# Kernel optimization log

Hardware: AMD Instinct MI355X
Metric: run time of the kernel (lower is better)

The kernel has to match this reference:

```python
import jax, jax.numpy as jnp
import numpy as np

N_HEADS = 16
EMBED = 1024
SEQ = 2048
BATCH = 4
GELU_C = 0.044715
EPS = 1e-5


def gelu_tanh(x):
    return 0.5 * x * (1.0 + jnp.tanh(jnp.sqrt(2.0 / jnp.pi) * (x + GELU_C * x ** 3)))


def layer_norm(x, scale, shift):
    mean = jnp.mean(x, axis=-1, keepdims=True)
    var = jnp.var(x, axis=-1, keepdims=True)
    return scale * (x - mean) / jnp.sqrt(var + EPS) + shift


def setup_inputs() -> dict:
    key = jax.random.key(0)
    ks = jax.random.split(key, 8)
    d = EMBED
    s = 0.02
    return {
        "X": jax.random.normal(ks[0], (BATCH, SEQ, d), dtype=jnp.float32),
        "Wq": jax.random.normal(ks[1], (d, d), dtype=jnp.float32) * s,
        "Wk": jax.random.normal(ks[2], (d, d), dtype=jnp.float32) * s,
        "Wv": jax.random.normal(ks[3], (d, d), dtype=jnp.float32) * s,
        "Wo": jax.random.normal(ks[4], (d, d), dtype=jnp.float32) * s,
        "W1": jax.random.normal(ks[5], (d, 4 * d), dtype=jnp.float32) * s,
        "b1": jnp.zeros((4 * d,), dtype=jnp.float32),
        "W2": jax.random.normal(ks[6], (4 * d, d), dtype=jnp.float32) * s,
        "b2": jnp.zeros((d,), dtype=jnp.float32),
        "ln1_scale": jnp.ones((d,), dtype=jnp.float32),
        "ln1_shift": jnp.zeros((d,), dtype=jnp.float32),
        "ln2_scale": jnp.ones((d,), dtype=jnp.float32),
        "ln2_shift": jnp.zeros((d,), dtype=jnp.float32),
    }


def attention(x, Wq, Wk, Wv, Wo):
    b, s, d = x.shape
    h, dh = N_HEADS, d // N_HEADS
    q = (x @ Wq).reshape(b, s, h, dh).transpose(0, 2, 1, 3)  # [b,h,s,dh]
    k = (x @ Wk).reshape(b, s, h, dh).transpose(0, 2, 1, 3)
    v = (x @ Wv).reshape(b, s, h, dh).transpose(0, 2, 1, 3)
    scores = jnp.einsum("bhqd,bhkd->bhqk", q, k) / jnp.sqrt(jnp.float32(dh))
    causal = jnp.tril(jnp.ones((s, s), dtype=bool))
    scores = jnp.where(causal, scores, -jnp.inf)
    w = jax.nn.softmax(scores, axis=-1)  # dropout rate 0 -> identity
    ctx = jnp.einsum("bhqk,bhkd->bhqd", w, v)
    ctx = ctx.transpose(0, 2, 1, 3).reshape(b, s, d)
    return ctx @ Wo


def reference(X, Wq, Wk, Wv, Wo, W1, b1, W2, b2,
              ln1_scale, ln1_shift, ln2_scale, ln2_shift):
    h = layer_norm(X, ln1_scale, ln1_shift)
    X = X + attention(h, Wq, Wk, Wv, Wo)
    h = layer_norm(X, ln2_scale, ln2_shift)
    h = gelu_tanh(h @ W1 + b1) @ W2 + b2
    return X + h
```

## Files before the change

### kernel.cpp

```cpp
#include <hip/hip_runtime.h>

typedef unsigned short u16;
typedef __attribute__((ext_vector_type(8))) short bf16x8;
typedef __attribute__((ext_vector_type(4))) float fx4;

#define MFMA16(a, b, c) __builtin_amdgcn_mfma_f32_16x16x32_bf16((a), (b), (c), 0, 0, 0)

__device__ __forceinline__ u16 f2bf(float f) {
  unsigned u = __float_as_uint(f);
  u += 0x7fffu + ((u >> 16) & 1u);
  return (u16)(u >> 16);
}

__device__ __forceinline__ void gload_lds16(const void* g, void* l) {
  __builtin_amdgcn_global_load_lds((const __attribute__((address_space(1))) void*)g,
                                   (__attribute__((address_space(3))) void*)l,
                                   16, 0, 0);
}

struct WP {
  const float* s[6];
  u16* d[6];
};
__global__ __launch_bounds__(256) void tcvt_all(WP p) {
  __shared__ float t[32][33];
  const int id = blockIdx.x;
  int which, bx, by, R, C;
  if (id < 4096) {
    which = id >> 10;
    const int q = id & 1023;
    bx = q >> 5; by = q & 31; R = 1024; C = 1024;
  } else if (id < 8192) {
    which = 4;
    const int q = id - 4096;
    bx = q & 127; by = q >> 7; R = 1024; C = 4096;
  } else {
    which = 5;
    const int q = id - 8192;
    bx = q & 31; by = q >> 5; R = 4096; C = 1024;
  }
  const float* src = p.s[which];
  u16* dst = p.d[which];
  const int tx = threadIdx.x & 31, ty = threadIdx.x >> 5;
#pragma unroll
  for (int i = 0; i < 4; ++i)
    t[ty + i * 8][tx] = src[(size_t)(by * 32 + ty + i * 8) * C + bx * 32 + tx];
  __syncthreads();
#pragma unroll
  for (int i = 0; i < 4; ++i)
    dst[(size_t)(bx * 32 + ty + i * 8) * R + by * 32 + tx] = f2bf(t[tx][ty + i * 8]);
}

__global__ __launch_bounds__(256) void ln_kernel(const float* __restrict__ x,
                                                 const float* __restrict__ sc,
                                                 const float* __restrict__ sh,
                                                 u16* __restrict__ out) {
  const int row = blockIdx.x, tid = threadIdx.x;
  const float4 v = ((const float4*)(x + (size_t)row * 1024))[tid];
  float s = v.x + v.y + v.z + v.w;
  float ss = v.x * v.x + v.y * v.y + v.z * v.z + v.w * v.w;
#pragma unroll
  for (int d = 32; d >= 1; d >>= 1) {
    s += __shfl_xor(s, d);
    ss += __shfl_xor(ss, d);
  }
  __shared__ float rs[4], rq[4];
  const int w = tid >> 6;
  if ((tid & 63) == 0) { rs[w] = s; rq[w] = ss; }
  __syncthreads();
  s = rs[0] + rs[1] + rs[2] + rs[3];
  ss = rq[0] + rq[1] + rq[2] + rq[3];
  const float mean = s * (1.f / 1024.f);
  const float var = ss * (1.f / 1024.f) - mean * mean;
  const float rstd = rsqrtf(var + 1e-5f);
  const float4 g = ((const float4*)sc)[tid];
  const float4 b = ((const float4*)sh)[tid];
  ushort4 o;
  o.x = f2bf(g.x * (v.x - mean) * rstd + b.x);
  o.y = f2bf(g.y * (v.y - mean) * rstd + b.y);
  o.z = f2bf(g.z * (v.z - mean) * rstd + b.z);
  o.w = f2bf(g.w * (v.w - mean) * rstd + b.w);
  ((ushort4*)(out + (size_t)row * 1024))[tid] = o;
}

__device__ __forceinline__ void xcd_map(int bid, int NTN, int& tMi, int& tNi) {
  const int xcd = bid & 7, i = bid >> 3;
  tMi = xcd + 8 * (i / NTN);
  tNi = i % NTN;
}

template <int MODE>
__global__ __launch_bounds__(256) void gemm_bf16(
    const u16* __restrict__ A, const u16* __restrict__ Bt, int K, int NTN,
    void* __restrict__ outp, const float* __restrict__ aux,
    u16* __restrict__ qd, u16* __restrict__ kd, u16* __restrict__ vd) {
  __shared__ u16 lA[128 * 32];
  __shared__ u16 lB[128 * 32];
  const int tid = threadIdx.x;
  const int w = tid >> 6, lane = tid & 63;
  const int lo = lane & 15, hi = lane >> 4;
  int tMi, tNi;
  xcd_map(blockIdx.x, NTN, tMi, tNi);
  const int tM = tMi * 128, tN = tNi * 128;
  const int wr = (w >> 1) << 6, wc = (w & 1) << 6;

  const u16 *sA[2], *sB[2];
  u16 *dA[2], *dB[2];
#pragma unroll
  for (int p = 0; p < 2; ++p) {
    const int c = p * 256 + tid;
    const int r = c >> 2, gs = (c & 3) ^ (r & 3);
    sA[p] = A + (size_t)(tM + r) * K + gs * 8;
    sB[p] = Bt + (size_t)(tN + r) * K + gs * 8;
    dA[p] = &lA[(p * 256 + w * 64) * 8];
    dB[p] = &lB[(p * 256 + w * 64) * 8];
  }

  fx4 acc[4][4];
#pragma unroll
  for (int m = 0; m < 4; ++m)
#pragma unroll
    for (int n = 0; n < 4; ++n) acc[m][n] = (fx4){0.f, 0.f, 0.f, 0.f};

  for (int kk = 0; kk < K; kk += 32) {
    __syncthreads();
#pragma unroll
    for (int p = 0; p < 2; ++p) {
      gload_lds16(sA[p] + kk, dA[p]);
      gload_lds16(sB[p] + kk, dB[p]);
    }
    __syncthreads();
    bf16x8 af[4], bfr[4];
#pragma unroll
    for (int m = 0; m < 4; ++m) {
      const int r = wr + m * 16 + lo;
      af[m] = *(const bf16x8*)&lA[r * 32 + ((hi ^ (r & 3)) << 3)];
    }
#pragma unroll
    for (int n = 0; n < 4; ++n) {
      const int r = wc + n * 16 + lo;
      bfr[n] = *(const bf16x8*)&lB[r * 32 + ((hi ^ (r & 3)) << 3)];
    }
#pragma unroll
    for (int m = 0; m < 4; ++m)
#pragma unroll
      for (int n = 0; n < 4; ++n) acc[m][n] = MFMA16(af[m], bfr[n], acc[m][n]);
  }

#pragma unroll
  for (int m = 0; m < 4; ++m) {
    const int rgb = tM + wr + m * 16 + hi * 4;
#pragma unroll
    for (int n = 0; n < 4; ++n) {
      const int cg = tN + wc + n * 16 + lo;
#pragma unroll
      for (int r = 0; r < 4; ++r) {
        const float v = acc[m][n][r];
        const int rg = rgb + r;
        if constexpr (MODE == 0) {
          const int which = cg >> 10, c = cg & 1023;
          const int head = c >> 6, dhi = c & 63;
          const int b = rg >> 11, sidx = rg & 2047;
          const int bh = b * 16 + head;
          const u16 bv = f2bf(v);
          if (which == 0)      qd[((size_t)bh * 2048 + sidx) * 64 + dhi] = bv;
          else if (which == 1) kd[((size_t)bh * 2048 + sidx) * 64 + dhi] = bv;
          else                 vd[((size_t)bh * 64 + dhi) * 2048 + sidx] = bv;
        } else if constexpr (MODE == 1) {
          float* o = (float*)outp;
          const size_t idx = (size_t)rg * 1024 + cg;
          o[idx] = aux[idx] + v;
        } else if constexpr (MODE == 2) {
          const float xx = v + aux[cg];
          const float t = xx + 0.044715f * xx * xx * xx;
          const float e = __expf(1.5957691216057308f * t);
          const float th = 1.f - 2.f / (e + 1.f);
          ((u16*)outp)[(size_t)rg * 4096 + cg] = f2bf(0.5f * xx * (1.f + th));
        } else {
          float* o = (float*)outp;
          const size_t idx = (size_t)rg * 1024 + cg;
          o[idx] = o[idx] + v + aux[cg];
        }
      }
    }
  }
}

__global__ __launch_bounds__(512) void attn_kernel(const u16* __restrict__ Q,
                                                   const u16* __restrict__ Kg,
                                                   const u16* __restrict__ Vt,
                                                   u16* __restrict__ ctx) {
  __shared__ u16 lK[2][64 * 64];
  __shared__ u16 lV[2][64 * 64];
  __shared__ u16 Plds[8][16 * 64];
  const int tid = threadIdx.x;
  const int w = tid >> 6, lane = tid & 63;
  const int lo = lane & 15, hi = lane >> 4;
  const int bh = blockIdx.x;
  const int j = blockIdx.y;
  const u16* Qb = Q + (size_t)bh * 2048 * 64;
  const u16* Kb = Kg + (size_t)bh * 2048 * 64;
  const u16* Vb = Vt + (size_t)bh * 64 * 2048;
  u16* Pw = Plds[w];
  const int nt0 = 2 * j + 2;

  const int rowS = tid >> 3;
  const int ugS = (tid & 7) ^ (rowS & 7);

#define STAGE(BUF, KB)                                                         \
  do {                                                                         \
    gload_lds16(Kb + (size_t)((KB) + rowS) * 64 + ugS * 8, &lK[BUF][tid * 8]); \
    gload_lds16(Vb + (size_t)rowS * 2048 + (KB) + ugS * 8, &lV[BUF][tid * 8]); \
  } while (0)

  const int b = bh >> 4, h = bh & 15;
  const float SCALE = 0.18033688011112042f;

  bf16x8 ones;
#pragma unroll
  for (int i = 0; i < 8; ++i) ones[i] = (short)0x3F80;

  int qt = j;
  int qw = qt * 128 + w * 16;

  bf16x8 qf[2];
#pragma unroll
  for (int kc = 0; kc < 2; ++kc)
    qf[kc] = *(const bf16x8*)&Qb[(size_t)(qw + lo) * 64 + kc * 32 + hi * 8];

  fx4 accO[4];
  fx4 accS = (fx4){0.f, 0.f, 0.f, 0.f};
#pragma unroll
  for (int t2 = 0; t2 < 4; ++t2) accO[t2] = (fx4){0.f, 0.f, 0.f, 0.f};

  STAGE(0, 0);
  __syncthreads();

  int buf = 0;
  for (int t = 0; t < 34; ++t) {
    if (t + 1 < 34) {
      const int tn = t + 1;
      const int kbn = (tn < nt0 ? tn : tn - nt0) * 64;
      STAGE(buf ^ 1, kbn);
    }
    if (t == nt0) {
#pragma unroll
      for (int t2 = 0; t2 < 4; ++t2)
#pragma unroll
        for (int r = 0; r < 4; ++r) {
          const int rg = b * 2048 + qw + hi * 4 + r;
          const int cg = h * 64 + t2 * 16 + lo;
          ctx[(size_t)rg * 1024 + cg] = f2bf(accO[t2][r] / accS[r]);
        }
      qt = 15 - j;
      qw = qt * 128 + w * 16;
#pragma unroll
      for (int kc = 0; kc < 2; ++kc)
        qf[kc] = *(const bf16x8*)&Qb[(size_t)(qw + lo) * 64 + kc * 32 + hi * 8];
#pragma unroll
      for (int t2 = 0; t2 < 4; ++t2) accO[t2] = (fx4){0.f, 0.f, 0.f, 0.f};
      accS = (fx4){0.f, 0.f, 0.f, 0.f};
    }
    const int kb = (t < nt0 ? t : t - nt0) * 64;
    if (kb <= qw + 15) {
      const u16* lKb = lK[buf];
      const u16* lVb = lV[buf];
      fx4 s[4];
#pragma unroll
      for (int tt = 0; tt < 4; ++tt) {
        const int r = tt * 16 + lo;
        const bf16x8 kf0 = *(const bf16x8*)&lKb[r * 64 + ((hi ^ (r & 7)) << 3)];
        const bf16x8 kf1 = *(const bf16x8*)&lKb[r * 64 + (((4 + hi) ^ (r & 7)) << 3)];
        fx4 z = (fx4){0.f, 0.f, 0.f, 0.f};
        z = MFMA16(qf[0], kf0, z);
        z = MFMA16(qf[1], kf1, z);
        s[tt] = z;
      }
      if (kb + 63 > qw) {
#pragma unroll
        for (int tt = 0; tt < 4; ++tt)
#pragma unroll
          for (int r = 0; r < 4; ++r) {
            const int key = kb + tt * 16 + lo;
            const int qr = qw + hi * 4 + r;
            s[tt][r] = (key > qr) ? 0.f : exp2f(s[tt][r] * SCALE);
          }
      } else {
#pragma unroll
        for (int tt = 0; tt < 4; ++tt)
#pragma unroll
          for (int r = 0; r < 4; ++r) s[tt][r] = exp2f(s[tt][r] * SCALE);
      }
#pragma unroll
      for (int r = 0; r < 4; ++r) {
        unsigned pk01, pk23;
        asm("v_cvt_pk_bf16_f32 %0, %1, %2" : "=v"(pk01) : "v"(s[0][r]), "v"(s[1][r]));
        asm("v_cvt_pk_bf16_f32 %0, %1, %2" : "=v"(pk23) : "v"(s[2][r]), "v"(s[3][r]));
        const int row = hi * 4 + r;
        const int sw = (row & 7) << 4;
        const int rbase = row * 128;
        Pw[(rbase + (((0 * 16 + lo) * 2) ^ sw)) >> 1] = (u16)pk01;
        Pw[(rbase + (((1 * 16 + lo) * 2) ^ sw)) >> 1] = (u16)(pk01 >> 16);
        Pw[(rbase + (((2 * 16 + lo) * 2) ^ sw)) >> 1] = (u16)pk23;
        Pw[(rbase + (((3 * 16 + lo) * 2) ^ sw)) >> 1] = (u16)(pk23 >> 16);
      }
      asm volatile("s_waitcnt lgkmcnt(0)" ::: "memory");
      bf16x8 pf[2];
#pragma unroll
      for (int kc = 0; kc < 2; ++kc) {
        const int row = lo;
        const int colB = kc * 64 + hi * 16;
        pf[kc] = *(const bf16x8*)((const char*)Pw + row * 128 + (colB ^ ((row & 7) << 4)));
      }
      accS = MFMA16(pf[0], ones, accS);
      accS = MFMA16(pf[1], ones, accS);
#pragma unroll
      for (int t2 = 0; t2 < 4; ++t2) {
        const int r2 = t2 * 16 + lo;
        const bf16x8 vf0 = *(const bf16x8*)&lVb[r2 * 64 + ((hi ^ (r2 & 7)) << 3)];
        const bf16x8 vf1 = *(const bf16x8*)&lVb[r2 * 64 + (((4 + hi) ^ (r2 & 7)) << 3)];
        accO[t2] = MFMA16(pf[0], vf0, accO[t2]);
        accO[t2] = MFMA16(pf[1], vf1, accO[t2]);
      }
    }
    __syncthreads();
    buf ^= 1;
  }
#pragma unroll
  for (int t2 = 0; t2 < 4; ++t2)
#pragma unroll
    for (int r = 0; r < 4; ++r) {
      const int rg = b * 2048 + qw + hi * 4 + r;
      const int cg = h * 64 + t2 * 16 + lo;
      ctx[(size_t)rg * 1024 + cg] = f2bf(accO[t2][r] / accS[r]);
    }
#undef STAGE
}

extern "C" void kernel_launch(void* const* d_in, const int* in_sizes, int n_in,
                              void* d_out, int out_size, void* d_ws, size_t ws_size,
                              hipStream_t stream) {
  const float* X    = (const float*)d_in[0];
  const float* Wq   = (const float*)d_in[1];
  const float* Wk   = (const float*)d_in[2];
  const float* Wv   = (const float*)d_in[3];
  const float* Wo   = (const float*)d_in[4];
  const float* W1   = (const float*)d_in[5];
  const float* b1   = (const float*)d_in[6];
  const float* W2   = (const float*)d_in[7];
  const float* b2   = (const float*)d_in[8];
  const float* ln1s = (const float*)d_in[9];
  const float* ln1b = (const float*)d_in[10];
  const float* ln2s = (const float*)d_in[11];
  const float* ln2b = (const float*)d_in[12];

  const size_t SZ_WQKVT = 3072UL * 1024;
  const size_t SZ_WOT   = 1024UL * 1024;
  const size_t SZ_W1T   = 4096UL * 1024;
  const size_t SZ_W2T   = 1024UL * 4096;
  const size_t SZ_H     = 8192UL * 1024;
  const size_t SZ_QKV   = 64UL * 2048 * 64;

  u16* WqkvT = (u16*)d_ws;
  u16* WoT   = WqkvT + SZ_WQKVT;
  u16* W1T   = WoT + SZ_WOT;
  u16* W2T   = W1T + SZ_W1T;
  u16* hbuf  = W2T + SZ_W2T;
  u16* qbuf  = hbuf + SZ_H;
  u16* kbuf  = qbuf + SZ_QKV;
  u16* vbuf  = kbuf + SZ_QKV;
  u16* gbuf  = vbuf + SZ_QKV;
  u16* ctx   = hbuf;
  u16* h2    = qbuf;

  float* out = (float*)d_out;
  dim3 blk(256);

  WP wp;
  wp.s[0] = Wq; wp.s[1] = Wk; wp.s[2] = Wv; wp.s[3] = Wo; wp.s[4] = W1; wp.s[5] = W2;
  wp.d[0] = WqkvT;
  wp.d[1] = WqkvT + 1024 * 1024;
  wp.d[2] = WqkvT + 2 * 1024 * 1024;
  wp.d[3] = WoT;
  wp.d[4] = W1T;
  wp.d[5] = W2T;
  tcvt_all<<<12288, blk, 0, stream>>>(wp);

  ln_kernel<<<8192, blk, 0, stream>>>(X, ln1s, ln1b, hbuf);
  gemm_bf16<0><<<1536, blk, 0, stream>>>(hbuf, WqkvT, 1024, 24,
                                         nullptr, nullptr, qbuf, kbuf, vbuf);
  attn_kernel<<<dim3(64, 8), dim3(512), 0, stream>>>(qbuf, kbuf, vbuf, ctx);
  gemm_bf16<1><<<512, blk, 0, stream>>>(ctx, WoT, 1024, 8,
                                        out, X, nullptr, nullptr, nullptr);
  ln_kernel<<<8192, blk, 0, stream>>>(out, ln2s, ln2b, h2);
  gemm_bf16<2><<<2048, blk, 0, stream>>>(h2, W1T, 1024, 32,
                                         gbuf, b1, nullptr, nullptr, nullptr);
  gemm_bf16<3><<<512, blk, 0, stream>>>(gbuf, W2T, 4096, 8,
                                        out, b2, nullptr, nullptr, nullptr);
}
```

Measured before the change: 452.5 us.

## Rewrite GEMM as triple-buffered 256x128 tile kernel with async LDS prefetch

Replaces the single-buffered 128x128, K=32 GEMM with a 512-thread kernel using 256x128 tiles, K=64 steps and three LDS stages. Global-to-LDS loads for tile t+2 are issued while tile t is computed, with one barrier per step and explicit vmcnt waits. The goal is to hide global load latency, halve the barriers per K, and raise data reuse per block. In exchange it uses roughly 144KB of LDS per block (one block per CU) and launches half as many blocks, which lowers occupancy and can leave CUs underused on the smaller GEMMs.

```diff
diff --git a/kernel.cpp b/kernel.cpp
--- a/kernel.cpp
+++ b/kernel.cpp
@@ -90,69 +90,92 @@
 }
 
 template <int MODE>
-__global__ __launch_bounds__(256) void gemm_bf16(
+__global__ __launch_bounds__(512, 1) void gemm3(
     const u16* __restrict__ A, const u16* __restrict__ Bt, int K, int NTN,
     void* __restrict__ outp, const float* __restrict__ aux,
     u16* __restrict__ qd, u16* __restrict__ kd, u16* __restrict__ vd) {
-  __shared__ u16 lA[128 * 32];
-  __shared__ u16 lB[128 * 32];
+  __shared__ u16 lA[3][256 * 64];
+  __shared__ u16 lB[3][128 * 64];
   const int tid = threadIdx.x;
-  const int w = tid >> 6, lane = tid & 63;
+  const int lane = tid & 63, w = tid >> 6;
   const int lo = lane & 15, hi = lane >> 4;
+  const int wm = w >> 1, wn = w & 1;
   int tMi, tNi;
   xcd_map(blockIdx.x, NTN, tMi, tNi);
-  const int tM = tMi * 128, tN = tNi * 128;
-  const int wr = (w >> 1) << 6, wc = (w & 1) << 6;
-
-  const u16 *sA[2], *sB[2];
-  u16 *dA[2], *dB[2];
-#pragma unroll
-  for (int p = 0; p < 2; ++p) {
-    const int c = p * 256 + tid;
-    const int r = c >> 2, gs = (c & 3) ^ (r & 3);
-    sA[p] = A + (size_t)(tM + r) * K + gs * 8;
-    sB[p] = Bt + (size_t)(tN + r) * K + gs * 8;
-    dA[p] = &lA[(p * 256 + w * 64) * 8];
-    dB[p] = &lB[(p * 256 + w * 64) * 8];
+  const int tM = tMi * 256, tN = tNi * 128;
+  const int NT = K >> 6;
+
+  const int rb = tid >> 3;
+  const int uc = ((tid & 7) ^ (rb & 7)) * 8;
+
+#define STAGE3(BUFI, KK)                                                 \
+  do {                                                                   \
+    _Pragma("unroll") for (int i = 0; i < 4; ++i) {                      \
+      gload_lds16(A + (size_t)(tM + i * 64 + rb) * K + (KK) + uc,        \
+                  &lA[BUFI][i * 4096 + tid * 8]);                        \
+    }                                                                    \
+    _Pragma("unroll") for (int i = 0; i < 2; ++i) {                      \
+      gload_lds16(Bt + (size_t)(tN + i * 64 + rb) * K + (KK) + uc,       \
+                  &lB[BUFI][i * 4096 + tid * 8]);                        \
+    }                                                                    \
+  } while (0)
+
+  fx4 acc[4][4];
+#pragma unroll
+  for (int m = 0; m < 4; ++m)
+#pragma unroll
+    for (int n = 0; n < 4; ++n) acc[m][n] = (fx4){0.f, 0.f, 0.f, 0.f};
+
+  STAGE3(0, 0);
+  STAGE3(1, 64);
+
+  int buf = 0;
+  for (int t = 0; t < NT; ++t) {
+    if (t < NT - 1) {
+      asm volatile("s_waitcnt vmcnt(6)" ::: "memory");
+    } else {
+      asm volatile("s_waitcnt vmcnt(0)" ::: "memory");
+    }
+    __builtin_amdgcn_sched_barrier(0);
+    __builtin_amdgcn_s_barrier();
+    __builtin_amdgcn_sched_barrier(0);
+    const int nbuf = buf + 2 >= 3 ? buf - 1 : buf + 2;
+    if (t + 2 < NT) STAGE3(nbuf, (t + 2) * 64);
+
+    const u16* bufA = &lA[buf][0];
+    const u16* bufB = &lB[buf][0];
+    bf16x8 af[4][2], bf[4][2];
+#pragma unroll
+    for (int m = 0; m < 4; ++m)
+#pragma unroll
+      for (int ks = 0; ks < 2; ++ks) {
+        const int R = wm * 64 + m * 16 + lo;
+        af[m][ks] = *(const bf16x8*)&bufA[R * 64 + (((ks << 2) + hi) ^ (R & 7)) * 8];
+      }
+#pragma unroll
+    for (int n = 0; n < 4; ++n)
+#pragma unroll
+      for (int ks = 0; ks < 2; ++ks) {
+        const int R = wn * 64 + n * 16 + lo;
+        bf[n][ks] = *(const bf16x8*)&bufB[R * 64 + (((ks << 2) + hi) ^ (R & 7)) * 8];
+      }
+#pragma unroll
+    for (int m = 0; m < 4; ++m)
+#pragma unroll
+      for (int n = 0; n < 4; ++n) {
+        acc[m][n] = MFMA16(af[m][0], bf[n][0], acc[m][n]);
+        acc[m][n] = MFMA16(af[m][1], bf[n][1], acc[m][n]);
+      }
+    buf = buf + 1 >= 3 ? 0 : buf + 1;
   }
-
-  fx4 acc[4][4];
-#pragma unroll
-  for (int m = 0; m < 4; ++m)
-#pragma unroll
-    for (int n = 0; n < 4; ++n) acc[m][n] = (fx4){0.f, 0.f, 0.f, 0.f};
-
-  for (int kk = 0; kk < K; kk += 32) {
-    __syncthreads();
-#pragma unroll
-    for (int p = 0; p < 2; ++p) {
-      gload_lds16(sA[p] + kk, dA[p]);
-      gload_lds16(sB[p] + kk, dB[p]);
-    }
-    __syncthreads();
-    bf16x8 af[4], bfr[4];
-#pragma unroll
-    for (int m = 0; m < 4; ++m) {
-      const int r = wr + m * 16 + lo;
-      af[m] = *(const bf16x8*)&lA[r * 32 + ((hi ^ (r & 3)) << 3)];
-    }
+#undef STAGE3
+
+#pragma unroll
+  for (int m = 0; m < 4; ++m) {
+    const int rgb = tM + wm * 64 + m * 16 + hi * 4;
 #pragma unroll
     for (int n = 0; n < 4; ++n) {
-      const int r = wc + n * 16 + lo;
-      bfr[n] = *(const bf16x8*)&lB[r * 32 + ((hi ^ (r & 3)) << 3)];
-    }
-#pragma unroll
-    for (int m = 0; m < 4; ++m)
-#pragma unroll
-      for (int n = 0; n < 4; ++n) acc[m][n] = MFMA16(af[m], bfr[n], acc[m][n]);
-  }
-
-#pragma unroll
-  for (int m = 0; m < 4; ++m) {
-    const int rgb = tM + wr + m * 16 + hi * 4;
-#pragma unroll
-    for (int n = 0; n < 4; ++n) {
-      const int cg = tN + wc + n * 16 + lo;
+      const int cg = tN + wn * 64 + n * 16 + lo;
 #pragma unroll
       for (int r = 0; r < 4; ++r) {
         const float v = acc[m][n][r];
@@ -172,8 +195,8 @@
           o[idx] = aux[idx] + v;
         } else if constexpr (MODE == 2) {
           const float xx = v + aux[cg];
-          const float t = xx + 0.044715f * xx * xx * xx;
-          const float e = __expf(1.5957691216057308f * t);
+          const float t2 = xx + 0.044715f * xx * xx * xx;
+          const float e = __expf(1.5957691216057308f * t2);
           const float th = 1.f - 2.f / (e + 1.f);
           ((u16*)outp)[(size_t)rg * 4096 + cg] = f2bf(0.5f * xx * (1.f + th));
         } else {
@@ -387,14 +410,14 @@
   tcvt_all<<<12288, blk, 0, stream>>>(wp);
 
   ln_kernel<<<8192, blk, 0, stream>>>(X, ln1s, ln1b, hbuf);
-  gemm_bf16<0><<<1536, blk, 0, stream>>>(hbuf, WqkvT, 1024, 24,
-                                         nullptr, nullptr, qbuf, kbuf, vbuf);
+  gemm3<0><<<768, dim3(512), 0, stream>>>(hbuf, WqkvT, 1024, 24,
+                                          nullptr, nullptr, qbuf, kbuf, vbuf);
   attn_kernel<<<dim3(64, 8), dim3(512), 0, stream>>>(qbuf, kbuf, vbuf, ctx);
-  gemm_bf16<1><<<512, blk, 0, stream>>>(ctx, WoT, 1024, 8,
-                                        out, X, nullptr, nullptr, nullptr);
+  gemm3<1><<<256, dim3(512), 0, stream>>>(ctx, WoT, 1024, 8,
+                                          out, X, nullptr, nullptr, nullptr);
   ln_kernel<<<8192, blk, 0, stream>>>(out, ln2s, ln2b, h2);
-  gemm_bf16<2><<<2048, blk, 0, stream>>>(h2, W1T, 1024, 32,
-                                         gbuf, b1, nullptr, nullptr, nullptr);
-  gemm_bf16<3><<<512, blk, 0, stream>>>(gbuf, W2T, 4096, 8,
-                                        out, b2, nullptr, nullptr, nullptr);
-}
+  gemm3<2><<<1024, dim3(512), 0, stream>>>(h2, W1T, 1024, 32,
+                                           gbuf, b1, nullptr, nullptr, nullptr);
+  gemm3<3><<<256, dim3(512), 0, stream>>>(gbuf, W2T, 4096, 8,
+                                          out, b2, nullptr, nullptr, nullptr);
+}
```

Result: faster. 424.1 us (-6.3%).

## Replace GEMM with 8-wave 256-row tiled, multi-buffered, phase-pipelined kernel

Applied to the files above, without the earlier changes.

Replaces the simple 128x128 single-buffered bf16 GEMM with a 512-thread kernel using 256xBN tiles (BN 128 or 256). It keeps four LDS stages of 32-wide K slices and issues global-to-LDS loads one phase ahead, with explicit vmcnt waits. The kernel also uses raw s_barrier, sched_barrier and setprio around the MFMA bursts. This targets the load latency and barrier stalls of the old loop and raises reuse per tile. In exchange LDS use is large (one block per CU), the 128-row grids shrink to 256 or 512 blocks (about one wave of blocks on 256 CUs), and correctness depends on the hand-counted waitcnts.

```diff
diff --git a/kernel.cpp b/kernel.cpp
--- a/kernel.cpp
+++ b/kernel.cpp
@@ -89,70 +89,129 @@
   tNi = i % NTN;
 }
 
-template <int MODE>
-__global__ __launch_bounds__(256) void gemm_bf16(
+template <int MODE, int BN>
+__global__ __launch_bounds__(512, 1) void gemm8p(
     const u16* __restrict__ A, const u16* __restrict__ Bt, int K, int NTN,
     void* __restrict__ outp, const float* __restrict__ aux,
     u16* __restrict__ qd, u16* __restrict__ kd, u16* __restrict__ vd) {
-  __shared__ u16 lA[128 * 32];
-  __shared__ u16 lB[128 * 32];
+  constexpr int WN = (BN == 256) ? 4 : 2;
+  constexpr int WM = 8 / WN;
+  constexpr int MR = 256 / (16 * WM);
+  constexpr int MR2 = MR / 2;
+  constexpr int BLOADS = BN / 128;
+  __shared__ u16 lA[2][2][256 * 32];
+  __shared__ u16 lB[2][2][BN * 32];
   const int tid = threadIdx.x;
-  const int w = tid >> 6, lane = tid & 63;
+  const int lane = tid & 63, w = tid >> 6;
   const int lo = lane & 15, hi = lane >> 4;
+  const int wm = w / WN, wn = w % WN;
   int tMi, tNi;
   xcd_map(blockIdx.x, NTN, tMi, tNi);
-  const int tM = tMi * 128, tN = tNi * 128;
-  const int wr = (w >> 1) << 6, wc = (w & 1) << 6;
-
-  const u16 *sA[2], *sB[2];
-  u16 *dA[2], *dB[2];
-#pragma unroll
-  for (int p = 0; p < 2; ++p) {
-    const int c = p * 256 + tid;
-    const int r = c >> 2, gs = (c & 3) ^ (r & 3);
-    sA[p] = A + (size_t)(tM + r) * K + gs * 8;
-    sB[p] = Bt + (size_t)(tN + r) * K + gs * 8;
-    dA[p] = &lA[(p * 256 + w * 64) * 8];
-    dB[p] = &lB[(p * 256 + w * 64) * 8];
-  }
-
-  fx4 acc[4][4];
-#pragma unroll
-  for (int m = 0; m < 4; ++m)
+  const int tM = tMi * 256, tN = tNi * BN;
+  const int NT = K >> 6;
+  const int NIT = K >> 7;
+
+#define STG_A(TI, KSH, GK)                                                       \
+  do {                                                                           \
+    _Pragma("unroll") for (int j = 0; j < 2; ++j) {                              \
+      const int idx = j * 512 + tid;                                             \
+      const int row = idx >> 2, u = idx & 3;                                     \
+      gload_lds16(A + (size_t)(tM + row) * K + (GK) + ((u ^ ((row >> 1) & 3)) * 8), \
+                  &lA[TI][KSH][idx * 8]);                                        \
+    }                                                                            \
+  } while (0)
+#define STG_B(TI, KSH, GK)                                                       \
+  do {                                                                           \
+    _Pragma("unroll") for (int j = 0; j < BLOADS; ++j) {                         \
+      const int idx = j * 512 + tid;                                             \
+      const int row = idx >> 2, u = idx & 3;                                     \
+      gload_lds16(Bt + (size_t)(tN + row) * K + (GK) + ((u ^ ((row >> 1) & 3)) * 8), \
+                  &lB[TI][KSH][idx * 8]);                                        \
+    }                                                                            \
+  } while (0)
+#define VMW                                                                      \
+  do {                                                                           \
+    if constexpr (BN == 256) asm volatile("s_waitcnt vmcnt(4)" ::: "memory");    \
+    else asm volatile("s_waitcnt vmcnt(3)" ::: "memory");                        \
+  } while (0)
+#define NOPS ((void)0)
+
+#define PHASE(P, STAGE_STMT, VM)                                                 \
+  {                                                                              \
+    constexpr int ksg = (P) >> 1;                                                \
+    constexpr int mh = (P) & 1;                                                  \
+    constexpr int ti = ksg >> 1;                                                 \
+    constexpr int ksh = ksg & 1;                                                 \
+    bf16x8 afr[MR2];                                                             \
+    _Pragma("unroll") for (int mi = 0; mi < MR2; ++mi) {                         \
+      const int R = wm * (MR * 16) + (mh * MR2 + mi) * 16 + lo;                  \
+      afr[mi] =                                                                  \
+          *(const bf16x8*)&lA[ti][ksh][R * 32 + ((hi ^ ((R >> 1) & 3)) * 8)];    \
+    }                                                                            \
+    if constexpr (mh == 0) {                                                     \
+      _Pragma("unroll") for (int n = 0; n < 4; ++n) {                            \
+        const int R = wn * 64 + n * 16 + lo;                                     \
+        bfr[n] =                                                                 \
+            *(const bf16x8*)&lB[ti][ksh][R * 32 + ((hi ^ ((R >> 1) & 3)) * 8)];  \
+      }                                                                          \
+    }                                                                            \
+    STAGE_STMT;                                                                  \
+    VM;                                                                          \
+    __builtin_amdgcn_s_barrier();                                                \
+    asm volatile("s_waitcnt lgkmcnt(0)" ::: "memory");                           \
+    __builtin_amdgcn_sched_barrier(0);                                           \
+    __builtin_amdgcn_s_setprio(1);                                               \
+    _Pragma("unroll") for (int mi = 0; mi < MR2; ++mi)                           \
+      _Pragma("unroll") for (int n = 0; n < 4; ++n)                              \
+        acc[mh * MR2 + mi][n] = MFMA16(afr[mi], bfr[n], acc[mh * MR2 + mi][n]);  \
+    __builtin_amdgcn_s_setprio(0);                                               \
+    __builtin_amdgcn_sched_barrier(0);                                           \
+    __builtin_amdgcn_s_barrier();                                                \
+    __builtin_amdgcn_sched_barrier(0);                                           \
+  }
+
+  fx4 acc[MR][4];
+#pragma unroll
+  for (int m = 0; m < MR; ++m)
 #pragma unroll
     for (int n = 0; n < 4; ++n) acc[m][n] = (fx4){0.f, 0.f, 0.f, 0.f};
-
-  for (int kk = 0; kk < K; kk += 32) {
-    __syncthreads();
-#pragma unroll
-    for (int p = 0; p < 2; ++p) {
-      gload_lds16(sA[p] + kk, dA[p]);
-      gload_lds16(sB[p] + kk, dB[p]);
-    }
-    __syncthreads();
-    bf16x8 af[4], bfr[4];
-#pragma unroll
-    for (int m = 0; m < 4; ++m) {
-      const int r = wr + m * 16 + lo;
-      af[m] = *(const bf16x8*)&lA[r * 32 + ((hi ^ (r & 3)) << 3)];
-    }
+  bf16x8 bfr[4];
+
+  STG_A(0, 0, 0);
+  STG_B(0, 0, 0);
+  STG_A(0, 1, 32);
+  STG_B(0, 1, 32);
+  STG_A(1, 0, 64);
+  STG_B(1, 0, 64);
+  if constexpr (BN == 256) asm volatile("s_waitcnt vmcnt(4)" ::: "memory");
+  else asm volatile("s_waitcnt vmcnt(3)" ::: "memory");
+  __builtin_amdgcn_s_barrier();
+  __builtin_amdgcn_sched_barrier(0);
+
+  for (int it = 0; it < NIT; ++it) {
+    const int t0 = 2 * it;
+    const bool g2 = (t0 + 2) < NT, g3 = (t0 + 3) < NT;
+    PHASE(0, STG_A(1, 1, (t0 + 1) * 64 + 32), NOPS)
+    PHASE(1, STG_B(1, 1, (t0 + 1) * 64 + 32), NOPS)
+    PHASE(2, if (g2) STG_A(0, 0, (t0 + 2) * 64), NOPS)
+    PHASE(3, if (g2) STG_B(0, 0, (t0 + 2) * 64), VMW)
+    PHASE(4, if (g2) STG_A(0, 1, (t0 + 2) * 64 + 32), NOPS)
+    PHASE(5, if (g2) STG_B(0, 1, (t0 + 2) * 64 + 32), NOPS)
+    PHASE(6, if (g3) STG_A(1, 0, (t0 + 3) * 64), NOPS)
+    PHASE(7, if (g3) STG_B(1, 0, (t0 + 3) * 64), VMW)
+  }
+#undef PHASE
+#undef STG_A
+#undef STG_B
+#undef VMW
+#undef NOPS
+
+#pragma unroll
+  for (int m = 0; m < MR; ++m) {
+    const int rgb = tM + wm * (MR * 16) + m * 16 + hi * 4;
 #pragma unroll
     for (int n = 0; n < 4; ++n) {
-      const int r = wc + n * 16 + lo;
-      bfr[n] = *(const bf16x8*)&lB[r * 32 + ((hi ^ (r & 3)) << 3)];
-    }
-#pragma unroll
-    for (int m = 0; m < 4; ++m)
-#pragma unroll
-      for (int n = 0; n < 4; ++n) acc[m][n] = MFMA16(af[m], bfr[n], acc[m][n]);
-  }
-
-#pragma unroll
-  for (int m = 0; m < 4; ++m) {
-    const int rgb = tM + wr + m * 16 + hi * 4;
-#pragma unroll
-    for (int n = 0; n < 4; ++n) {
-      const int cg = tN + wc + n * 16 + lo;
+      const int cg = tN + wn * 64 + n * 16 + lo;
 #pragma unroll
       for (int r = 0; r < 4; ++r) {
         const float v = acc[m][n][r];
@@ -172,8 +231,8 @@
           o[idx] = aux[idx] + v;
         } else if constexpr (MODE == 2) {
           const float xx = v + aux[cg];
-          const float t = xx + 0.044715f * xx * xx * xx;
-          const float e = __expf(1.5957691216057308f * t);
+          const float t2 = xx + 0.044715f * xx * xx * xx;
+          const float e = __expf(1.5957691216057308f * t2);
           const float th = 1.f - 2.f / (e + 1.f);
           ((u16*)outp)[(size_t)rg * 4096 + cg] = f2bf(0.5f * xx * (1.f + th));
         } else {
@@ -387,14 +446,14 @@
   tcvt_all<<<12288, blk, 0, stream>>>(wp);
 
   ln_kernel<<<8192, blk, 0, stream>>>(X, ln1s, ln1b, hbuf);
-  gemm_bf16<0><<<1536, blk, 0, stream>>>(hbuf, WqkvT, 1024, 24,
-                                         nullptr, nullptr, qbuf, kbuf, vbuf);
+  gemm8p<0, 128><<<768, dim3(512), 0, stream>>>(hbuf, WqkvT, 1024, 24,
+                                                nullptr, nullptr, qbuf, kbuf, vbuf);
   attn_kernel<<<dim3(64, 8), dim3(512), 0, stream>>>(qbuf, kbuf, vbuf, ctx);
-  gemm_bf16<1><<<512, blk, 0, stream>>>(ctx, WoT, 1024, 8,
-                                        out, X, nullptr, nullptr, nullptr);
+  gemm8p<1, 128><<<256, dim3(512), 0, stream>>>(ctx, WoT, 1024, 8,
+                                                out, X, nullptr, nullptr, nullptr);
   ln_kernel<<<8192, blk, 0, stream>>>(out, ln2s, ln2b, h2);
-  gemm_bf16<2><<<2048, blk, 0, stream>>>(h2, W1T, 1024, 32,
-                                         gbuf, b1, nullptr, nullptr, nullptr);
-  gemm_bf16<3><<<512, blk, 0, stream>>>(gbuf, W2T, 4096, 8,
-                                        out, b2, nullptr, nullptr, nullptr);
-}
+  gemm8p<2, 256><<<512, dim3(512), 0, stream>>>(h2, W1T, 1024, 16,
+                                                gbuf, b1, nullptr, nullptr, nullptr);
+  gemm8p<3, 128><<<256, dim3(512), 0, stream>>>(gbuf, W2T, 4096, 8,
+                                                out, b2, nullptr, nullptr, nullptr);
+}
```

Measured after the change: 414.2 us. 8.5% less time.
